# Kernel tuning notes

Hardware: AMD Instinct MI355X
Metric: run time of the kernel (lower is better)

The kernel has to match this reference:

```python
import math
import jax, jax.numpy as jnp
import numpy as np

M = 0.4
H = 0.333
S = 64.0
T_ALPHA = 1.0
EPS = 1e-3
BM0 = 20.0   # initial batch_mean buffer
BS0 = 100.0  # initial batch_std buffer


def setup_inputs() -> dict:
    key = jax.random.key(0)
    k1, k2, k3 = jax.random.split(key, 3)
    N, C = 2048, 50000
    cosine = jax.random.uniform(k1, (N, C), dtype=jnp.float32)  # in [0,1) subset of valid cosine range
    norms = jax.random.uniform(k2, (N, 1), dtype=jnp.float32)
    label = jax.random.randint(k3, (N,), 0, C, dtype=jnp.int64)
    return {"cosine": cosine, "norms": norms, "label": label}


def reference(cosine, norms, label):
    N, C = cosine.shape
    valid = (label != -1)                      # rows that get a margin (partial-FC)
    validf = valid.astype(cosine.dtype)

    # norm statistics are detached in the original (clone().detach())
    safe_norms = jax.lax.stop_gradient(jnp.clip(norms, 1e-3, 100.0))
    mean = safe_norms.mean()
    std = jnp.std(safe_norms, ddof=1)          # torch .std() is unbiased
    batch_mean = mean * T_ALPHA + (1.0 - T_ALPHA) * BM0
    batch_std = std * T_ALPHA + (1.0 - T_ALPHA) * BS0

    margin_scaler = jnp.clip((safe_norms - batch_mean) / (batch_std + EPS) * H, -1.0, 1.0)[:, 0]  # [N]

    rows = jnp.arange(N)
    lab = jnp.where(valid, label, 0)

    # angular margin: add g_angular at the label column, then clip full positive rows
    theta = jnp.arccos(cosine)                 # [N, C]
    g_angular = -M * margin_scaler * validf    # [N]
    theta = theta.at[rows, lab].add(g_angular)
    theta = jnp.where(valid[:, None], jnp.clip(theta, EPS, math.pi - EPS), theta)
    cos_m = jnp.cos(theta)

    # additive margin at the label column
    g_add = (M + M * margin_scaler) * validf   # [N]
    cos_m = cos_m.at[rows, lab].add(-g_add)

    return cos_m * S
```

## Files before the change

### kernel.cpp

```cpp
#include <hip/hip_runtime.h>
#include <math.h>


#define MARGIN    0.4f
#define HPARAM    0.333f
#define SCALE     64.0f
#define EPSF      1e-3f
#define COS_EPS   0.999999500000041653f
#define PI_M_EPS  3.140592653589793f

__global__ __launch_bounds__(256) void stats_kernel(const float* __restrict__ norms,
                                                    int N, float* __restrict__ ws) {
    __shared__ double sdata[256];
    const int t = threadIdx.x;

    double s = 0.0;
    for (int i = t; i < N; i += 256) {
        float v = fminf(fmaxf(norms[i], 1e-3f), 100.0f);
        s += (double)v;
    }
    sdata[t] = s;
    __syncthreads();
    for (int k = 128; k > 0; k >>= 1) {
        if (t < k) sdata[t] += sdata[t + k];
        __syncthreads();
    }
    const double mean = sdata[0] / (double)N;
    __syncthreads();

    double sq = 0.0;
    for (int i = t; i < N; i += 256) {
        float v = fminf(fmaxf(norms[i], 1e-3f), 100.0f);
        double d = (double)v - mean;
        sq += d * d;
    }
    sdata[t] = sq;
    __syncthreads();
    for (int k = 128; k > 0; k >>= 1) {
        if (t < k) sdata[t] += sdata[t + k];
        __syncthreads();
    }
    if (t == 0) {
        ws[0] = (float)mean;
        ws[1] = (float)sqrt(sdata[0] / (double)(N - 1));
    }
}

__global__ __launch_bounds__(256) void adaface_kernel(
        const float* __restrict__ cosine,
        const float* __restrict__ norms,
        const int*   __restrict__ label,
        const float* __restrict__ ws,
        float*       __restrict__ out,
        int C) {
    const int row  = blockIdx.y;
    const int c4   = blockIdx.x * blockDim.x + threadIdx.x;
    const int base = c4 * 4;
    if (base >= C) return;

    const int  lab   = label[row];
    const bool valid = (lab != -1);

    const size_t off = (size_t)row * (size_t)C + (size_t)base;
    const float4 x = *reinterpret_cast<const float4*>(cosine + off);
    float4 y;

    if (valid) {
        y.x = fminf(fmaxf(x.x, -COS_EPS), COS_EPS) * SCALE;
        y.y = fminf(fmaxf(x.y, -COS_EPS), COS_EPS) * SCALE;
        y.z = fminf(fmaxf(x.z, -COS_EPS), COS_EPS) * SCALE;
        y.w = fminf(fmaxf(x.w, -COS_EPS), COS_EPS) * SCALE;

        if (lab >= base && lab < base + 4) {
            const float bm = ws[0];
            const float bs = ws[1];
            const float sn = fminf(fmaxf(norms[row], 1e-3f), 100.0f);
            const float ms = fminf(fmaxf((sn - bm) / (bs + EPSF) * HPARAM, -1.0f), 1.0f);

            const int k = lab - base;
            const float xv = (&x.x)[k];
            float theta = acosf(xv) - MARGIN * ms;
            theta = fminf(fmaxf(theta, EPSF), PI_M_EPS);
            const float g_add = MARGIN + MARGIN * ms;
            (&y.x)[k] = (cosf(theta) - g_add) * SCALE;
        }
    } else {
        y.x = x.x * SCALE;
        y.y = x.y * SCALE;
        y.z = x.z * SCALE;
        y.w = x.w * SCALE;
    }

    *reinterpret_cast<float4*>(out + off) = y;
}

extern "C" void kernel_launch(void* const* d_in, const int* in_sizes, int n_in,
                              void* d_out, int out_size, void* d_ws, size_t ws_size,
                              hipStream_t stream) {
    const float* cosine = (const float*)d_in[0];
    const float* norms  = (const float*)d_in[1];
    const int*   label  = (const int*)d_in[2];
    float*       out    = (float*)d_out;
    float*       ws     = (float*)d_ws;

    const int N = in_sizes[2];
    const int C = in_sizes[0] / N;

    stats_kernel<<<1, 256, 0, stream>>>(norms, N, ws);

    const int c4      = (C + 3) / 4;
    const int gx      = (c4 + 255) / 256;
    dim3 grid(gx, N, 1);
    adaface_kernel<<<grid, 256, 0, stream>>>(cosine, norms, label, ws, out, C);
}
```

Baseline: 187.8 us.

## Precompute per-row label fix in prep kernel; row-per-block streaming with nontemporal accesses

The single-block stats kernel now also computes the margin-adjusted label value for every row and stores it in the workspace. The main kernel switches to one block per row that loops over the columns, using nontemporal vector loads and stores and substituting the precomputed value at the label column. This removes per-thread label branches and the acos/cos from the hot kernel and is meant to cut cache pollution on the streaming traffic. In exchange it adds serial work to the one-block prep kernel and gives each block a long column loop, and C4=C/4 silently drops any tail when C is not a multiple of 4.

```diff
diff --git a/kernel.cpp b/kernel.cpp
--- a/kernel.cpp
+++ b/kernel.cpp
@@ -9,8 +9,13 @@
 #define COS_EPS   0.999999500000041653f
 #define PI_M_EPS  3.140592653589793f
 
-__global__ __launch_bounds__(256) void stats_kernel(const float* __restrict__ norms,
-                                                    int N, float* __restrict__ ws) {
+typedef float f32x4 __attribute__((ext_vector_type(4)));
+
+__global__ __launch_bounds__(256) void prep_kernel(const float* __restrict__ norms,
+                                                   const int*   __restrict__ label,
+                                                   const float* __restrict__ cosine,
+                                                   int N, int C,
+                                                   float* __restrict__ ws) {
     __shared__ double sdata[256];
     const int t = threadIdx.x;
 
@@ -40,58 +45,65 @@
         if (t < k) sdata[t] += sdata[t + k];
         __syncthreads();
     }
-    if (t == 0) {
-        ws[0] = (float)mean;
-        ws[1] = (float)sqrt(sdata[0] / (double)(N - 1));
+    const float bm = (float)mean;
+    const float bs = (float)sqrt(sdata[0] / (double)(N - 1));
+    if (t == 0) { ws[0] = bm; ws[1] = bs; }
+    __syncthreads();
+
+    for (int row = t; row < N; row += 256) {
+        const int lab = label[row];
+        float fix = 0.0f;
+        if (lab != -1) {
+            const float sn = fminf(fmaxf(norms[row], 1e-3f), 100.0f);
+            const float ms = fminf(fmaxf((sn - bm) / (bs + EPSF) * HPARAM, -1.0f), 1.0f);
+            const float xv = cosine[(size_t)row * (size_t)C + (size_t)lab];
+            float theta = acosf(xv) - MARGIN * ms;
+            theta = fminf(fmaxf(theta, EPSF), PI_M_EPS);
+            fix = (cosf(theta) - (MARGIN + MARGIN * ms)) * SCALE;
+        }
+        ws[2 + row] = fix;
     }
 }
 
-__global__ __launch_bounds__(256) void adaface_kernel(
+__global__ __launch_bounds__(256) void adaface_main(
         const float* __restrict__ cosine,
-        const float* __restrict__ norms,
         const int*   __restrict__ label,
         const float* __restrict__ ws,
         float*       __restrict__ out,
-        int C) {
-    const int row  = blockIdx.y;
-    const int c4   = blockIdx.x * blockDim.x + threadIdx.x;
-    const int base = c4 * 4;
-    if (base >= C) return;
+        int C4) {
+    const int row = blockIdx.x;
+    const int lab = label[row];
+    const bool valid = (lab != -1);
+    const int lab4 = lab >> 2;
+    const int labk = lab & 3;
+    const float fix = ws[2 + row];
 
-    const int  lab   = label[row];
-    const bool valid = (lab != -1);
-
-    const size_t off = (size_t)row * (size_t)C + (size_t)base;
-    const float4 x = *reinterpret_cast<const float4*>(cosine + off);
-    float4 y;
+    const f32x4* __restrict__ src = reinterpret_cast<const f32x4*>(cosine) + (size_t)row * (size_t)C4;
+    f32x4*       __restrict__ dst = reinterpret_cast<f32x4*>(out)          + (size_t)row * (size_t)C4;
 
     if (valid) {
-        y.x = fminf(fmaxf(x.x, -COS_EPS), COS_EPS) * SCALE;
-        y.y = fminf(fmaxf(x.y, -COS_EPS), COS_EPS) * SCALE;
-        y.z = fminf(fmaxf(x.z, -COS_EPS), COS_EPS) * SCALE;
-        y.w = fminf(fmaxf(x.w, -COS_EPS), COS_EPS) * SCALE;
-
-        if (lab >= base && lab < base + 4) {
-            const float bm = ws[0];
-            const float bs = ws[1];
-            const float sn = fminf(fmaxf(norms[row], 1e-3f), 100.0f);
-            const float ms = fminf(fmaxf((sn - bm) / (bs + EPSF) * HPARAM, -1.0f), 1.0f);
-
-            const int k = lab - base;
-            const float xv = (&x.x)[k];
-            float theta = acosf(xv) - MARGIN * ms;
-            theta = fminf(fmaxf(theta, EPSF), PI_M_EPS);
-            const float g_add = MARGIN + MARGIN * ms;
-            (&y.x)[k] = (cosf(theta) - g_add) * SCALE;
+        for (int c4 = threadIdx.x; c4 < C4; c4 += 256) {
+            f32x4 x = __builtin_nontemporal_load(src + c4);
+            f32x4 y;
+            y.x = fminf(fmaxf(x.x, -COS_EPS), COS_EPS) * SCALE;
+            y.y = fminf(fmaxf(x.y, -COS_EPS), COS_EPS) * SCALE;
+            y.z = fminf(fmaxf(x.z, -COS_EPS), COS_EPS) * SCALE;
+            y.w = fminf(fmaxf(x.w, -COS_EPS), COS_EPS) * SCALE;
+            if (c4 == lab4) {
+                y.x = (labk == 0) ? fix : y.x;
+                y.y = (labk == 1) ? fix : y.y;
+                y.z = (labk == 2) ? fix : y.z;
+                y.w = (labk == 3) ? fix : y.w;
+            }
+            __builtin_nontemporal_store(y, dst + c4);
         }
     } else {
-        y.x = x.x * SCALE;
-        y.y = x.y * SCALE;
-        y.z = x.z * SCALE;
-        y.w = x.w * SCALE;
+        for (int c4 = threadIdx.x; c4 < C4; c4 += 256) {
+            f32x4 x = __builtin_nontemporal_load(src + c4);
+            f32x4 y = { x.x * SCALE, x.y * SCALE, x.z * SCALE, x.w * SCALE };
+            __builtin_nontemporal_store(y, dst + c4);
+        }
     }
-
-    *reinterpret_cast<float4*>(out + off) = y;
 }
 
 extern "C" void kernel_launch(void* const* d_in, const int* in_sizes, int n_in,
@@ -103,13 +115,10 @@
     float*       out    = (float*)d_out;
     float*       ws     = (float*)d_ws;
 
-    const int N = in_sizes[2];
-    const int C = in_sizes[0] / N;
+    const int N  = in_sizes[2];
+    const int C  = in_sizes[0] / N;
+    const int C4 = C / 4;
 
-    stats_kernel<<<1, 256, 0, stream>>>(norms, N, ws);
-
-    const int c4      = (C + 3) / 4;
-    const int gx      = (c4 + 255) / 256;
-    dim3 grid(gx, N, 1);
-    adaface_kernel<<<grid, 256, 0, stream>>>(cosine, norms, label, ws, out, C);
+    prep_kernel<<<1, 256, 0, stream>>>(norms, label, cosine, N, C, ws);
+    adaface_main<<<N, 256, 0, stream>>>(cosine, label, ws, out, C4);
 }
```

New measurement: 185.9 us. No clear change (-1.0%).
